# Performance work log

Hardware: AMD Instinct MI355X
Metric: run time of the kernel (lower is better)

Reference implementation:

```python
import jax, jax.numpy as jnp
import numpy as np

EPS = 1e-06
H = 25  # num heads


def _rmsnorm(x, w, eps=EPS):
    # normalize over last dim in float32, as in the torch module
    xf = x.astype(jnp.float32)
    var = jnp.mean(xf * xf, axis=-1, keepdims=True)
    return (w * (xf * jax.lax.rsqrt(var + eps))).astype(x.dtype)


def setup_inputs() -> dict:
    key = jax.random.key(0)
    ks = jax.random.split(key, 4)
    B, N, C = 8, 1025, 3200
    x = jax.random.normal(ks[0], (B, N, C), dtype=jnp.float32)
    qkv_w = jax.random.normal(ks[1], (C, 3 * C), dtype=jnp.float32) * (C ** -0.5)
    qkv_b = jnp.zeros((3 * C,), dtype=jnp.float32)
    q_norm_w = jnp.ones((C,), dtype=jnp.float32)
    k_norm_w = jnp.ones((C,), dtype=jnp.float32)
    proj_w = jax.random.normal(ks[2], (C, C), dtype=jnp.float32) * (C ** -0.5)
    proj_b = jnp.zeros((C,), dtype=jnp.float32)
    return {"x": x, "qkv_w": qkv_w, "qkv_b": qkv_b, "q_norm_w": q_norm_w,
            "k_norm_w": k_norm_w, "proj_w": proj_w, "proj_b": proj_b}


def reference(x, qkv_w, qkv_b, q_norm_w, k_norm_w, proj_w, proj_b):
    B, N, C = x.shape
    D = C // H
    scale = D ** -0.5
    qkv = x @ qkv_w + qkv_b                      # [B, N, 3C]
    q, k, v = jnp.split(qkv, 3, axis=-1)         # each [B, N, C]
    # QK RMSNorm is over the FULL embed_dim (heads flattened), per source.
    q = _rmsnorm(q, q_norm_w)
    k = _rmsnorm(k, k_norm_w)
    q = q.reshape(B, N, H, D)
    k = k.reshape(B, N, H, D)
    v = v.reshape(B, N, H, D)
    attn = jnp.einsum('bqhd,bkhd->bhqk', q * scale, k)   # [B, H, N, N]
    attn = jax.nn.softmax(attn, axis=-1)
    out = jnp.einsum('bhqk,bkhd->bqhd', attn, v).reshape(B, N, C)
    return out @ proj_w + proj_b
```

## Files before the change

kernel.cpp:

```cpp
#include <hip/hip_runtime.h>
#include <hip/hip_bf16.h>
#include <math.h>

#define B_ 8
#define N_ 1025
#define C_ 3200
#define H_ 25
#define D_ 128
#define M_ (B_ * N_)
#define C3_ (3 * C_)

typedef unsigned short u16;
typedef unsigned int u32;
typedef short bf16x8 __attribute__((ext_vector_type(8)));
typedef float f32x4 __attribute__((ext_vector_type(4)));

__device__ inline void load_lds16(const void* g, void* s) {
    __builtin_amdgcn_global_load_lds(
        (const __attribute__((address_space(1))) void*)g,
        (__attribute__((address_space(3))) void*)s, 16, 0, 0);
}

__device__ inline void split_pair(float x0, float x1, u32& hpk, u32& lpk) {
    __hip_bfloat162 h2 = __float22bfloat162_rn(float2{x0, x1});
    union { __hip_bfloat162 b; u32 u; } cv; cv.b = h2;
    u32 h = cv.u;
    float hf0 = __uint_as_float(h << 16);
    float hf1 = __uint_as_float(h & 0xFFFF0000u);
    __hip_bfloat162 l2 = __float22bfloat162_rn(float2{x0 - hf0, x1 - hf1});
    union { __hip_bfloat162 b; u32 u; } cl; cl.b = l2;
    hpk = h; lpk = cl.u;
}

__device__ inline void split1(float x, u16& h, u16& l) {
    union { __hip_bfloat16 b; u16 u; } ch, cl;
    ch.b = __float2bfloat16(x);
    float hf = __uint_as_float(((u32)ch.u) << 16);
    cl.b = __float2bfloat16(x - hf);
    h = ch.u; l = cl.u;
}

__global__ __launch_bounds__(256) void convert_split(
    const float4* __restrict__ in, uint2* __restrict__ hi,
    uint2* __restrict__ lo, int n4)
{
    int i = blockIdx.x * 256 + threadIdx.x;
    if (i < n4) {
        float4 v = in[i];
        u32 h0, l0, h1, l1;
        split_pair(v.x, v.y, h0, l0);
        split_pair(v.z, v.w, h1, l1);
        hi[i] = make_uint2(h0, h1);
        lo[i] = make_uint2(l0, l1);
    }
}

__global__ __launch_bounds__(256) void convert_tsplit(
    const float* __restrict__ in, u16* __restrict__ hi, u16* __restrict__ lo,
    int K, int Nn)
{
    __shared__ float T[32][33];
    const int tid = threadIdx.x;
    const int nb = blockIdx.x * 32, kb = blockIdx.y * 32;
    #pragma unroll
    for (int p = 0; p < 4; ++p) {
        int k = p * 8 + (tid >> 5), n = tid & 31;
        T[k][n] = in[(size_t)(kb + k) * Nn + nb + n];
    }
    __syncthreads();
    const int nn = tid >> 3, k0 = (tid & 7) * 4;
    u32 h0, l0, h1, l1;
    split_pair(T[k0][nn], T[k0 + 1][nn], h0, l0);
    split_pair(T[k0 + 2][nn], T[k0 + 3][nn], h1, l1);
    size_t o = (size_t)(nb + nn) * K + kb + k0;
    *(uint2*)&hi[o] = make_uint2(h0, h1);
    *(uint2*)&lo[o] = make_uint2(l0, l1);
}

__global__ __launch_bounds__(256) void gemm_bf16split(
    const u16* __restrict__ Ah, const u16* __restrict__ Al,
    const u16* __restrict__ Bh, const u16* __restrict__ Bl,
    const float* __restrict__ bias, float* __restrict__ Cc,
    int M, int N)
{
    __shared__ u16 As_h[4][128][8];
    __shared__ u16 As_l[4][128][8];
    __shared__ u16 Bs_h[4][128][8];
    __shared__ u16 Bs_l[4][128][8];

    const int tid  = threadIdx.x;
    const int lane = tid & 63;
    const int w    = tid >> 6;
    const int wm   = w & 1, wn = w >> 1;
    const int lr = lane & 15, lg = lane >> 4;

    const int gX   = gridDim.x;
    const int nwg  = gX * gridDim.y;
    const int orig = blockIdx.y * gX + blockIdx.x;
    const int q8 = nwg >> 3, r8 = nwg & 7;
    const int xcd = orig & 7, oi = orig >> 3;
    const int wg = (xcd < r8 ? xcd * (q8 + 1)
                             : r8 * (q8 + 1) + (xcd - r8) * q8) + oi;
    const int rowBase = (wg / gX) * 128;
    const int colBase = (wg % gX) * 128;

    f32x4 acc[4][4] = {};

    for (int k0 = 0; k0 < C_; k0 += 32) {
        #pragma unroll
        for (int p = 0; p < 2; ++p) {
            int c   = p * 256 + tid;
            int row = c & 127, kc = c >> 7;
            int ldsOff = (p * 256 + w * 64) * 8;
            int ar = rowBase + row; if (ar >= M) ar = M - 1;
            size_t aoff = (size_t)ar * C_ + k0 + kc * 8;
            size_t boff = (size_t)(colBase + row) * C_ + k0 + kc * 8;
            load_lds16(Ah + aoff, (u16*)As_h + ldsOff);
            load_lds16(Al + aoff, (u16*)As_l + ldsOff);
            load_lds16(Bh + boff, (u16*)Bs_h + ldsOff);
            load_lds16(Bl + boff, (u16*)Bs_l + ldsOff);
        }
        __syncthreads();

        bf16x8 ah[4], al[4], bh[4], bl[4];
        #pragma unroll
        for (int i = 0; i < 4; ++i) {
            ah[i] = *(const bf16x8*)&As_h[lg][wm * 64 + i * 16 + lr][0];
            al[i] = *(const bf16x8*)&As_l[lg][wm * 64 + i * 16 + lr][0];
            bh[i] = *(const bf16x8*)&Bs_h[lg][wn * 64 + i * 16 + lr][0];
            bl[i] = *(const bf16x8*)&Bs_l[lg][wn * 64 + i * 16 + lr][0];
        }

        #pragma unroll
        for (int j = 0; j < 4; ++j)
            #pragma unroll
            for (int i = 0; i < 4; ++i)
                acc[i][j] = __builtin_amdgcn_mfma_f32_16x16x32_bf16(
                    ah[i], bh[j], acc[i][j], 0, 0, 0);
        #pragma unroll
        for (int j = 0; j < 4; ++j)
            #pragma unroll
            for (int i = 0; i < 4; ++i)
                acc[i][j] = __builtin_amdgcn_mfma_f32_16x16x32_bf16(
                    al[i], bh[j], acc[i][j], 0, 0, 0);
        #pragma unroll
        for (int j = 0; j < 4; ++j)
            #pragma unroll
            for (int i = 0; i < 4; ++i)
                acc[i][j] = __builtin_amdgcn_mfma_f32_16x16x32_bf16(
                    ah[i], bl[j], acc[i][j], 0, 0, 0);
        __syncthreads();
    }

    #pragma unroll
    for (int i = 0; i < 4; ++i) {
        #pragma unroll
        for (int j = 0; j < 4; ++j) {
            int gc = colBase + wn * 64 + j * 16 + lr;
            float bv = bias[gc];
            #pragma unroll
            for (int r = 0; r < 4; ++r) {
                int gr = rowBase + wm * 64 + i * 16 + lg * 4 + r;
                if (gr < M) Cc[(size_t)gr * N + gc] = acc[i][j][r] + bv;
            }
        }
    }
}

__global__ __launch_bounds__(256) void gemm_split(
    const float* __restrict__ A, const float* __restrict__ Bm,
    const float* __restrict__ bias, float* __restrict__ Cc,
    int M, int N)
{
    __shared__ u16  As_hi[128 * 32];
    __shared__ u16  As_lo[128 * 32];
    __shared__ float Bf[32 * 128];

    const int tid  = threadIdx.x;
    const int lane = tid & 63;
    const int w    = tid >> 6;
    const int wm   = w & 1, wn = w >> 1;
    const int rowBase = blockIdx.y * 128;
    const int colBase = blockIdx.x * 128;
    const int lr = lane & 15, lg = lane >> 4;

    const int ar = tid >> 3;
    const int ak = (tid & 7) * 4;

    f32x4 acc[4][4] = {};

    for (int k0 = 0; k0 < C_; k0 += 32) {
        #pragma unroll
        for (int p = 0; p < 4; ++p) {
            int c = p * 256 + tid;
            const float* g = Bm + (size_t)(k0 + (c >> 5)) * N
                                + colBase + (c & 31) * 4;
            load_lds16(g, &Bf[(p * 256 + w * 64) * 4]);
        }
        #pragma unroll
        for (int p = 0; p < 4; ++p) {
            int r  = p * 32 + ar;
            int gr = rowBase + r; if (gr >= M) gr = M - 1;
            float4 a4 = *(const float4*)(A + (size_t)gr * C_ + k0 + ak);
            u32 h0, h1, l0, l1;
            split_pair(a4.x, a4.y, h0, l0);
            split_pair(a4.z, a4.w, h1, l1);
            *(uint2*)&As_hi[r * 32 + ak] = make_uint2(h0, h1);
            *(uint2*)&As_lo[r * 32 + ak] = make_uint2(l0, l1);
        }
        __syncthreads();

        bf16x8 ah[4], al[4];
        #pragma unroll
        for (int i = 0; i < 4; ++i) {
            ah[i] = *(const bf16x8*)&As_hi[(wm * 64 + i * 16 + lr) * 32 + lg * 8];
            al[i] = *(const bf16x8*)&As_lo[(wm * 64 + i * 16 + lr) * 32 + lg * 8];
        }
        #pragma unroll
        for (int j = 0; j < 4; ++j) {
            const float* bp = &Bf[(lg * 8) * 128 + wn * 64 + j * 16 + lr];
            union { u32 u[4]; bf16x8 v; } BH, BL;
            split_pair(bp[0 * 128], bp[1 * 128], BH.u[0], BL.u[0]);
            split_pair(bp[2 * 128], bp[3 * 128], BH.u[1], BL.u[1]);
            split_pair(bp[4 * 128], bp[5 * 128], BH.u[2], BL.u[2]);
            split_pair(bp[6 * 128], bp[7 * 128], BH.u[3], BL.u[3]);
            #pragma unroll
            for (int i = 0; i < 4; ++i)
                acc[i][j] = __builtin_amdgcn_mfma_f32_16x16x32_bf16(
                    ah[i], BH.v, acc[i][j], 0, 0, 0);
            #pragma unroll
            for (int i = 0; i < 4; ++i)
                acc[i][j] = __builtin_amdgcn_mfma_f32_16x16x32_bf16(
                    al[i], BH.v, acc[i][j], 0, 0, 0);
            #pragma unroll
            for (int i = 0; i < 4; ++i)
                acc[i][j] = __builtin_amdgcn_mfma_f32_16x16x32_bf16(
                    ah[i], BL.v, acc[i][j], 0, 0, 0);
        }
        __syncthreads();
    }

    #pragma unroll
    for (int i = 0; i < 4; ++i) {
        #pragma unroll
        for (int j = 0; j < 4; ++j) {
            int gc = colBase + wn * 64 + j * 16 + lr;
            float bv = bias[gc];
            #pragma unroll
            for (int r = 0; r < 4; ++r) {
                int gr = rowBase + wm * 64 + i * 16 + lg * 4 + r;
                if (gr < M) Cc[(size_t)gr * N + gc] = acc[i][j][r] + bv;
            }
        }
    }
}

__global__ __launch_bounds__(256) void rmsnorm_kernel(
    float* __restrict__ qkv, const float* __restrict__ qw,
    const float* __restrict__ kw)
{
    const int row   = blockIdx.x >> 1;
    const int which = blockIdx.x & 1;
    float* p = qkv + (size_t)row * C3_ + which * C_;
    const float* w = which ? kw : qw;
    const int tid = threadIdx.x;

    float ss = 0.f;
    for (int i = tid; i < C_ / 4; i += 256) {
        float4 v = ((const float4*)p)[i];
        ss += v.x * v.x + v.y * v.y + v.z * v.z + v.w * v.w;
    }
    #pragma unroll
    for (int off = 32; off; off >>= 1) ss += __shfl_down(ss, off);

    __shared__ float wsum[4];
    __shared__ float stot;
    if ((tid & 63) == 0) wsum[tid >> 6] = ss;
    __syncthreads();
    if (tid == 0) stot = wsum[0] + wsum[1] + wsum[2] + wsum[3];
    __syncthreads();

    const float scale = rsqrtf(stot / (float)C_ + 1e-6f);
    for (int i = tid; i < C_ / 4; i += 256) {
        float4 v  = ((const float4*)p)[i];
        float4 wv = ((const float4*)w)[i];
        v.x *= scale * wv.x; v.y *= scale * wv.y;
        v.z *= scale * wv.z; v.w *= scale * wv.w;
        ((float4*)p)[i] = v;
    }
}

__global__ __launch_bounds__(256, 2) void flash_mfma(
    const float* __restrict__ qkv, float* __restrict__ attn_out)
{
    __shared__ u16 Kh[4][32][32];
    __shared__ u16 Kl[4][32][32];
    __shared__ u16 Vth[128][40];
    __shared__ u16 Vtl[128][40];
    __shared__ u16 Ph[4][16][40];
    __shared__ u16 Pl[4][16][40];

    const int b   = blockIdx.z;
    const int h   = blockIdx.y;
    const int q0  = blockIdx.x * 64;
    const int tid = threadIdx.x;
    const int lane = tid & 63;
    const int w    = tid >> 6;
    const int lr = lane & 15, lg = lane >> 4;
    const float scale = 0.088388347648318447f;

    bf16x8 qh[4], ql[4];
    {
        int qr = q0 + w * 16 + lr;
        if (qr >= N_) qr = N_ - 1;
        const float* qp = qkv + (size_t)(b * N_ + qr) * C3_ + h * D_;
        #pragma unroll
        for (int c = 0; c < 4; ++c) {
            float4 x0 = *(const float4*)(qp + c * 32 + lg * 8);
            float4 x1 = *(const float4*)(qp + c * 32 + lg * 8 + 4);
            union { u32 u[4]; bf16x8 v; } Hq, Lq;
            split_pair(x0.x * scale, x0.y * scale, Hq.u[0], Lq.u[0]);
            split_pair(x0.z * scale, x0.w * scale, Hq.u[1], Lq.u[1]);
            split_pair(x1.x * scale, x1.y * scale, Hq.u[2], Lq.u[2]);
            split_pair(x1.z * scale, x1.w * scale, Hq.u[3], Lq.u[3]);
            qh[c] = Hq.v; ql[c] = Lq.v;
        }
    }

    const float* Kbase = qkv + (size_t)b * N_ * C3_ + C_ + h * D_;
    const float* Vbase = qkv + (size_t)b * N_ * C3_ + 2 * C_ + h * D_;

    const int skr = tid >> 3;
    const int skd = (tid & 7) * 16;
    const int svk = (tid & 15) * 2;
    const int svd = (tid >> 4) * 4;

    float4 kg[4], vg[2][2];

    auto stage_load = [&](int kt) {
        int kk = kt * 32 + skr;
        if (kk < N_) {
            const float* p = Kbase + (size_t)kk * C3_ + skd;
            kg[0] = *(const float4*)(p + 0);
            kg[1] = *(const float4*)(p + 4);
            kg[2] = *(const float4*)(p + 8);
            kg[3] = *(const float4*)(p + 12);
        } else {
            kg[0] = kg[1] = kg[2] = kg[3] = make_float4(0.f, 0.f, 0.f, 0.f);
        }
        #pragma unroll
        for (int r = 0; r < 2; ++r) {
            int vk = kt * 32 + svk + r;
            if (vk < N_) {
                const float* p = Vbase + (size_t)vk * C3_ + svd;
                vg[0][r] = *(const float4*)(p);
                vg[1][r] = *(const float4*)(p + 64);
            } else {
                vg[0][r] = make_float4(0.f, 0.f, 0.f, 0.f);
                vg[1][r] = make_float4(0.f, 0.f, 0.f, 0.f);
            }
        }
    };

    auto stage_store = [&]() {
        #pragma unroll
        for (int i = 0; i < 4; ++i) {
            int d = skd + i * 4;
            int c = d >> 5, dd = d & 31;
            u32 h0, l0, h1, l1;
            split_pair(kg[i].x, kg[i].y, h0, l0);
            split_pair(kg[i].z, kg[i].w, h1, l1);
            *(uint2*)&Kh[c][skr][dd] = make_uint2(h0, h1);
            *(uint2*)&Kl[c][skr][dd] = make_uint2(l0, l1);
        }
        #pragma unroll
        for (int half = 0; half < 2; ++half) {
            float a0[4] = { vg[half][0].x, vg[half][0].y, vg[half][0].z, vg[half][0].w };
            float a1[4] = { vg[half][1].x, vg[half][1].y, vg[half][1].z, vg[half][1].w };
            #pragma unroll
            for (int i = 0; i < 4; ++i) {
                int d = svd + half * 64 + i;
                u32 hp, lp;
                split_pair(a0[i], a1[i], hp, lp);
                *(u32*)&Vth[d][svk] = hp;
                *(u32*)&Vtl[d][svk] = lp;
            }
        }
    };

    f32x4 oacc[8] = {};
    float m[4]    = { -INFINITY, -INFINITY, -INFINITY, -INFINITY };
    float lsum[4] = { 0.f, 0.f, 0.f, 0.f };

    const int nkt = (N_ + 31) / 32;
    stage_load(0);
    for (int kt = 0; kt < nkt; ++kt) {
        __syncthreads();
        stage_store();
        __syncthreads();
        if (kt + 1 < nkt) stage_load(kt + 1);

        f32x4 s0 = {}, s1 = {};
        #pragma unroll
        for (int c = 0; c < 4; ++c) {
            bf16x8 kh0 = *(const bf16x8*)&Kh[c][lr][lg * 8];
            bf16x8 kl0 = *(const bf16x8*)&Kl[c][lr][lg * 8];
            bf16x8 kh1 = *(const bf16x8*)&Kh[c][16 + lr][lg * 8];
            bf16x8 kl1 = *(const bf16x8*)&Kl[c][16 + lr][lg * 8];
            s0 = __builtin_amdgcn_mfma_f32_16x16x32_bf16(qh[c], kh0, s0, 0, 0, 0);
            s0 = __builtin_amdgcn_mfma_f32_16x16x32_bf16(ql[c], kh0, s0, 0, 0, 0);
            s0 = __builtin_amdgcn_mfma_f32_16x16x32_bf16(qh[c], kl0, s0, 0, 0, 0);
            s1 = __builtin_amdgcn_mfma_f32_16x16x32_bf16(qh[c], kh1, s1, 0, 0, 0);
            s1 = __builtin_amdgcn_mfma_f32_16x16x32_bf16(ql[c], kh1, s1, 0, 0, 0);
            s1 = __builtin_amdgcn_mfma_f32_16x16x32_bf16(qh[c], kl1, s1, 0, 0, 0);
        }

        const int kb = kt * 32;
        const bool v0 = (kb + lr) < N_;
        const bool v1 = (kb + 16 + lr) < N_;
        #pragma unroll
        for (int r = 0; r < 4; ++r) {
            if (!v0) s0[r] = -INFINITY;
            if (!v1) s1[r] = -INFINITY;
        }

        #pragma unroll
        for (int r = 0; r < 4; ++r) {
            float mt = fmaxf(s0[r], s1[r]);
            mt = fmaxf(mt, __shfl_xor(mt, 1));
            mt = fmaxf(mt, __shfl_xor(mt, 2));
            mt = fmaxf(mt, __shfl_xor(mt, 4));
            mt = fmaxf(mt, __shfl_xor(mt, 8));
            float mn = fmaxf(m[r], mt);
            float al = __expf(m[r] - mn);
            m[r] = mn;
            float p0 = __expf(s0[r] - mn);
            float p1 = __expf(s1[r] - mn);
            float ls = p0 + p1;
            ls += __shfl_xor(ls, 1);
            ls += __shfl_xor(ls, 2);
            ls += __shfl_xor(ls, 4);
            ls += __shfl_xor(ls, 8);
            lsum[r] = lsum[r] * al + ls;
            #pragma unroll
            for (int dt = 0; dt < 8; ++dt) oacc[dt][r] *= al;

            u16 hh, ll;
            split1(p0, hh, ll);
            Ph[w][lg * 4 + r][lr] = hh;
            Pl[w][lg * 4 + r][lr] = ll;
            split1(p1, hh, ll);
            Ph[w][lg * 4 + r][16 + lr] = hh;
            Pl[w][lg * 4 + r][16 + lr] = ll;
        }

        bf16x8 pah = *(const bf16x8*)&Ph[w][lr][lg * 8];
        bf16x8 pal = *(const bf16x8*)&Pl[w][lr][lg * 8];
        #pragma unroll
        for (int dt = 0; dt < 8; ++dt) {
            bf16x8 vh = *(const bf16x8*)&Vth[dt * 16 + lr][lg * 8];
            bf16x8 vl = *(const bf16x8*)&Vtl[dt * 16 + lr][lg * 8];
            oacc[dt] = __builtin_amdgcn_mfma_f32_16x16x32_bf16(pah, vh, oacc[dt], 0, 0, 0);
            oacc[dt] = __builtin_amdgcn_mfma_f32_16x16x32_bf16(pal, vh, oacc[dt], 0, 0, 0);
            oacc[dt] = __builtin_amdgcn_mfma_f32_16x16x32_bf16(pah, vl, oacc[dt], 0, 0, 0);
        }
    }

    #pragma unroll
    for (int r = 0; r < 4; ++r) {
        int q = q0 + w * 16 + lg * 4 + r;
        if (q < N_) {
            float inv = 1.f / lsum[r];
            float* op = attn_out + (size_t)(b * N_ + q) * C_ + h * D_ + lr;
            #pragma unroll
            for (int dt = 0; dt < 8; ++dt) op[dt * 16] = oacc[dt][r] * inv;
        }
    }
}

extern "C" void kernel_launch(void* const* d_in, const int* in_sizes, int n_in,
                              void* d_out, int out_size, void* d_ws, size_t ws_size,
                              hipStream_t stream)
{
    const float* x        = (const float*)d_in[0];
    const float* qkv_w    = (const float*)d_in[1];
    const float* qkv_b    = (const float*)d_in[2];
    const float* q_norm_w = (const float*)d_in[3];
    const float* k_norm_w = (const float*)d_in[4];
    const float* proj_w   = (const float*)d_in[5];
    const float* proj_b   = (const float*)d_in[6];
    float* out = (float*)d_out;

    const size_t fQ = (size_t)M_ * C3_;
    const size_t fA = (size_t)M_ * C_;
    const size_t uW = (size_t)C3_ * C_;

    float* qkv      = (float*)d_ws;
    float* attn_out = qkv + fQ;

    const size_t need = (fQ + fA) * 4 + fA * 2 * 2 + uW * 2 * 2;

    dim3 blk(256);

    if (ws_size >= need) {
        u16* xh = (u16*)(attn_out + fA);
        u16* xl = xh + fA;
        u16* wh = xl + fA;
        u16* wl = wh + uW;

        const int n4 = (int)(fA / 4);

        convert_split<<<dim3((n4 + 255) / 256), blk, 0, stream>>>(
            (const float4*)x, (uint2*)xh, (uint2*)xl, n4);
        convert_tsplit<<<dim3(C3_ / 32, C_ / 32), blk, 0, stream>>>(
            qkv_w, wh, wl, C_, C3_);

        gemm_bf16split<<<dim3(C3_ / 128, (M_ + 127) / 128), blk, 0, stream>>>(
            xh, xl, wh, wl, qkv_b, qkv, M_, C3_);

        rmsnorm_kernel<<<dim3(M_ * 2), blk, 0, stream>>>(qkv, q_norm_w, k_norm_w);

        flash_mfma<<<dim3((N_ + 63) / 64, H_, B_), blk, 0, stream>>>(qkv, attn_out);

        convert_split<<<dim3((n4 + 255) / 256), blk, 0, stream>>>(
            (const float4*)attn_out, (uint2*)xh, (uint2*)xl, n4);
        convert_tsplit<<<dim3(C_ / 32, C_ / 32), blk, 0, stream>>>(
            proj_w, wh, wl, C_, C_);

        gemm_bf16split<<<dim3(C_ / 128, (M_ + 127) / 128), blk, 0, stream>>>(
            xh, xl, wh, wl, proj_b, out, M_, C_);
    } else {
        gemm_split<<<dim3(C3_ / 128, (M_ + 127) / 128), blk, 0, stream>>>(
            x, qkv_w, qkv_b, qkv, M_, C3_);
        rmsnorm_kernel<<<dim3(M_ * 2), blk, 0, stream>>>(qkv, q_norm_w, k_norm_w);
        flash_mfma<<<dim3((N_ + 63) / 64, H_, B_), blk, 0, stream>>>(qkv, attn_out);
        gemm_split<<<dim3(C_ / 128, (M_ + 127) / 128), blk, 0, stream>>>(
            attn_out, proj_w, proj_b, out, M_, C_);
    }
}
```

Measured before the change: 3.999 ms.

## Fuse input bf16 split into QKV GEMM and emit split attention output directly

The QKV GEMM now reads fp32 x and splits it into hi/lo bf16 in registers while loading it into LDS, prefetching the next k-slice, which removes the separate convert pass over x. The QKV weight is converted and multiplied in three C-wide chunks so the workspace only needs one CxC split buffer. The flash kernel writes the hi/lo bf16 split of its output directly, dropping the fp32 attention buffer and its convert kernel. The proj weight split reuses the start of the qkv workspace, which is dead after attention, and the small-workspace fallback path is removed. The cost is more launches, x being re-read and re-split three times, and a hard dependence on a minimum workspace size.

```diff
diff --git a/kernel.cpp b/kernel.cpp
--- a/kernel.cpp
+++ b/kernel.cpp
@@ -40,24 +40,9 @@
     h = ch.u; l = cl.u;
 }
 
-__global__ __launch_bounds__(256) void convert_split(
-    const float4* __restrict__ in, uint2* __restrict__ hi,
-    uint2* __restrict__ lo, int n4)
-{
-    int i = blockIdx.x * 256 + threadIdx.x;
-    if (i < n4) {
-        float4 v = in[i];
-        u32 h0, l0, h1, l1;
-        split_pair(v.x, v.y, h0, l0);
-        split_pair(v.z, v.w, h1, l1);
-        hi[i] = make_uint2(h0, h1);
-        lo[i] = make_uint2(l0, l1);
-    }
-}
-
 __global__ __launch_bounds__(256) void convert_tsplit(
     const float* __restrict__ in, u16* __restrict__ hi, u16* __restrict__ lo,
-    int K, int Nn)
+    int K, int Nn, int strideN)
 {
     __shared__ float T[32][33];
     const int tid = threadIdx.x;
@@ -65,7 +50,7 @@
     #pragma unroll
     for (int p = 0; p < 4; ++p) {
         int k = p * 8 + (tid >> 5), n = tid & 31;
-        T[k][n] = in[(size_t)(kb + k) * Nn + nb + n];
+        T[k][n] = in[(size_t)(kb + k) * strideN + nb + n];
     }
     __syncthreads();
     const int nn = tid >> 3, k0 = (tid & 7) * 4;
@@ -77,11 +62,11 @@
     *(uint2*)&lo[o] = make_uint2(l0, l1);
 }
 
-__global__ __launch_bounds__(256) void gemm_bf16split(
-    const u16* __restrict__ Ah, const u16* __restrict__ Al,
+__global__ __launch_bounds__(256) void gemm_asplit(
+    const float* __restrict__ A,
     const u16* __restrict__ Bh, const u16* __restrict__ Bl,
     const float* __restrict__ bias, float* __restrict__ Cc,
-    int M, int N)
+    int M, int N, int ldc)
 {
     __shared__ u16 As_h[4][128][8];
     __shared__ u16 As_l[4][128][8];
@@ -104,12 +89,124 @@
     const int rowBase = (wg / gX) * 128;
     const int colBase = (wg % gX) * 128;
 
+    const int arow = tid >> 1;
+    const int akh  = (tid & 1) * 16;
+    const int kc0  = akh >> 3;
+    int gr0 = rowBase + arow; if (gr0 >= M) gr0 = M - 1;
+    const float* aptr = A + (size_t)gr0 * C_ + akh;
+
     f32x4 acc[4][4] = {};
 
+    float4 a0 = *(const float4*)(aptr + 0);
+    float4 a1 = *(const float4*)(aptr + 4);
+    float4 a2 = *(const float4*)(aptr + 8);
+    float4 a3 = *(const float4*)(aptr + 12);
+
     for (int k0 = 0; k0 < C_; k0 += 32) {
         #pragma unroll
         for (int p = 0; p < 2; ++p) {
-            int c   = p * 256 + tid;
+            int c = p * 256 + tid;
+            int row = c & 127, kc = c >> 7;
+            int ldsOff = (p * 256 + w * 64) * 8;
+            size_t boff = (size_t)(colBase + row) * C_ + k0 + kc * 8;
+            load_lds16(Bh + boff, (u16*)Bs_h + ldsOff);
+            load_lds16(Bl + boff, (u16*)Bs_l + ldsOff);
+        }
+        u32 h0,h1,h2,h3,h4,h5,h6,h7, l0,l1,l2,l3,l4,l5,l6,l7;
+        split_pair(a0.x, a0.y, h0, l0); split_pair(a0.z, a0.w, h1, l1);
+        split_pair(a1.x, a1.y, h2, l2); split_pair(a1.z, a1.w, h3, l3);
+        split_pair(a2.x, a2.y, h4, l4); split_pair(a2.z, a2.w, h5, l5);
+        split_pair(a3.x, a3.y, h6, l6); split_pair(a3.z, a3.w, h7, l7);
+        *(uint4*)&As_h[kc0][arow][0]     = make_uint4(h0, h1, h2, h3);
+        *(uint4*)&As_h[kc0 + 1][arow][0] = make_uint4(h4, h5, h6, h7);
+        *(uint4*)&As_l[kc0][arow][0]     = make_uint4(l0, l1, l2, l3);
+        *(uint4*)&As_l[kc0 + 1][arow][0] = make_uint4(l4, l5, l6, l7);
+        if (k0 + 32 < C_) {
+            const float* ap = aptr + k0 + 32;
+            a0 = *(const float4*)(ap + 0);
+            a1 = *(const float4*)(ap + 4);
+            a2 = *(const float4*)(ap + 8);
+            a3 = *(const float4*)(ap + 12);
+        }
+        __syncthreads();
+
+        bf16x8 ah[4], al[4], bh[4], bl[4];
+        #pragma unroll
+        for (int i = 0; i < 4; ++i) {
+            ah[i] = *(const bf16x8*)&As_h[lg][wm * 64 + i * 16 + lr][0];
+            al[i] = *(const bf16x8*)&As_l[lg][wm * 64 + i * 16 + lr][0];
+            bh[i] = *(const bf16x8*)&Bs_h[lg][wn * 64 + i * 16 + lr][0];
+            bl[i] = *(const bf16x8*)&Bs_l[lg][wn * 64 + i * 16 + lr][0];
+        }
+        #pragma unroll
+        for (int j = 0; j < 4; ++j)
+            #pragma unroll
+            for (int i = 0; i < 4; ++i)
+                acc[i][j] = __builtin_amdgcn_mfma_f32_16x16x32_bf16(
+                    ah[i], bh[j], acc[i][j], 0, 0, 0);
+        #pragma unroll
+        for (int j = 0; j < 4; ++j)
+            #pragma unroll
+            for (int i = 0; i < 4; ++i)
+                acc[i][j] = __builtin_amdgcn_mfma_f32_16x16x32_bf16(
+                    al[i], bh[j], acc[i][j], 0, 0, 0);
+        #pragma unroll
+        for (int j = 0; j < 4; ++j)
+            #pragma unroll
+            for (int i = 0; i < 4; ++i)
+                acc[i][j] = __builtin_amdgcn_mfma_f32_16x16x32_bf16(
+                    ah[i], bl[j], acc[i][j], 0, 0, 0);
+        __syncthreads();
+    }
+
+    #pragma unroll
+    for (int i = 0; i < 4; ++i) {
+        #pragma unroll
+        for (int j = 0; j < 4; ++j) {
+            int gc = colBase + wn * 64 + j * 16 + lr;
+            float bv = bias[gc];
+            #pragma unroll
+            for (int r = 0; r < 4; ++r) {
+                int gr = rowBase + wm * 64 + i * 16 + lg * 4 + r;
+                if (gr < M) Cc[(size_t)gr * ldc + gc] = acc[i][j][r] + bv;
+            }
+        }
+    }
+}
+
+__global__ __launch_bounds__(256) void gemm_bf16split(
+    const u16* __restrict__ Ah, const u16* __restrict__ Al,
+    const u16* __restrict__ Bh, const u16* __restrict__ Bl,
+    const float* __restrict__ bias, float* __restrict__ Cc,
+    int M, int N, int ldc)
+{
+    __shared__ u16 As_h[4][128][8];
+    __shared__ u16 As_l[4][128][8];
+    __shared__ u16 Bs_h[4][128][8];
+    __shared__ u16 Bs_l[4][128][8];
+
+    const int tid  = threadIdx.x;
+    const int lane = tid & 63;
+    const int w    = tid >> 6;
+    const int wm   = w & 1, wn = w >> 1;
+    const int lr = lane & 15, lg = lane >> 4;
+
+    const int gX   = gridDim.x;
+    const int nwg  = gX * gridDim.y;
+    const int orig = blockIdx.y * gX + blockIdx.x;
+    const int q8 = nwg >> 3, r8 = nwg & 7;
+    const int xcd = orig & 7, oi = orig >> 3;
+    const int wg = (xcd < r8 ? xcd * (q8 + 1)
+                             : r8 * (q8 + 1) + (xcd - r8) * q8) + oi;
+    const int rowBase = (wg / gX) * 128;
+    const int colBase = (wg % gX) * 128;
+
+    f32x4 acc[4][4] = {};
+
+    for (int k0 = 0; k0 < C_; k0 += 32) {
+        #pragma unroll
+        for (int p = 0; p < 2; ++p) {
+            int c = p * 256 + tid;
             int row = c & 127, kc = c >> 7;
             int ldsOff = (p * 256 + w * 64) * 8;
             int ar = rowBase + row; if (ar >= M) ar = M - 1;
@@ -130,7 +227,6 @@
             bh[i] = *(const bf16x8*)&Bs_h[lg][wn * 64 + i * 16 + lr][0];
             bl[i] = *(const bf16x8*)&Bs_l[lg][wn * 64 + i * 16 + lr][0];
         }
-
         #pragma unroll
         for (int j = 0; j < 4; ++j)
             #pragma unroll
@@ -161,95 +257,7 @@
             #pragma unroll
             for (int r = 0; r < 4; ++r) {
                 int gr = rowBase + wm * 64 + i * 16 + lg * 4 + r;
-                if (gr < M) Cc[(size_t)gr * N + gc] = acc[i][j][r] + bv;
-            }
-        }
-    }
-}
-
-__global__ __launch_bounds__(256) void gemm_split(
-    const float* __restrict__ A, const float* __restrict__ Bm,
-    const float* __restrict__ bias, float* __restrict__ Cc,
-    int M, int N)
-{
-    __shared__ u16  As_hi[128 * 32];
-    __shared__ u16  As_lo[128 * 32];
-    __shared__ float Bf[32 * 128];
-
-    const int tid  = threadIdx.x;
-    const int lane = tid & 63;
-    const int w    = tid >> 6;
-    const int wm   = w & 1, wn = w >> 1;
-    const int rowBase = blockIdx.y * 128;
-    const int colBase = blockIdx.x * 128;
-    const int lr = lane & 15, lg = lane >> 4;
-
-    const int ar = tid >> 3;
-    const int ak = (tid & 7) * 4;
-
-    f32x4 acc[4][4] = {};
-
-    for (int k0 = 0; k0 < C_; k0 += 32) {
-        #pragma unroll
-        for (int p = 0; p < 4; ++p) {
-            int c = p * 256 + tid;
-            const float* g = Bm + (size_t)(k0 + (c >> 5)) * N
-                                + colBase + (c & 31) * 4;
-            load_lds16(g, &Bf[(p * 256 + w * 64) * 4]);
-        }
-        #pragma unroll
-        for (int p = 0; p < 4; ++p) {
-            int r  = p * 32 + ar;
-            int gr = rowBase + r; if (gr >= M) gr = M - 1;
-            float4 a4 = *(const float4*)(A + (size_t)gr * C_ + k0 + ak);
-            u32 h0, h1, l0, l1;
-            split_pair(a4.x, a4.y, h0, l0);
-            split_pair(a4.z, a4.w, h1, l1);
-            *(uint2*)&As_hi[r * 32 + ak] = make_uint2(h0, h1);
-            *(uint2*)&As_lo[r * 32 + ak] = make_uint2(l0, l1);
-        }
-        __syncthreads();
-
-        bf16x8 ah[4], al[4];
-        #pragma unroll
-        for (int i = 0; i < 4; ++i) {
-            ah[i] = *(const bf16x8*)&As_hi[(wm * 64 + i * 16 + lr) * 32 + lg * 8];
-            al[i] = *(const bf16x8*)&As_lo[(wm * 64 + i * 16 + lr) * 32 + lg * 8];
-        }
-        #pragma unroll
-        for (int j = 0; j < 4; ++j) {
-            const float* bp = &Bf[(lg * 8) * 128 + wn * 64 + j * 16 + lr];
-            union { u32 u[4]; bf16x8 v; } BH, BL;
-            split_pair(bp[0 * 128], bp[1 * 128], BH.u[0], BL.u[0]);
-            split_pair(bp[2 * 128], bp[3 * 128], BH.u[1], BL.u[1]);
-            split_pair(bp[4 * 128], bp[5 * 128], BH.u[2], BL.u[2]);
-            split_pair(bp[6 * 128], bp[7 * 128], BH.u[3], BL.u[3]);
-            #pragma unroll
-            for (int i = 0; i < 4; ++i)
-                acc[i][j] = __builtin_amdgcn_mfma_f32_16x16x32_bf16(
-                    ah[i], BH.v, acc[i][j], 0, 0, 0);
-            #pragma unroll
-            for (int i = 0; i < 4; ++i)
-                acc[i][j] = __builtin_amdgcn_mfma_f32_16x16x32_bf16(
-                    al[i], BH.v, acc[i][j], 0, 0, 0);
-            #pragma unroll
-            for (int i = 0; i < 4; ++i)
-                acc[i][j] = __builtin_amdgcn_mfma_f32_16x16x32_bf16(
-                    ah[i], BL.v, acc[i][j], 0, 0, 0);
-        }
-        __syncthreads();
-    }
-
-    #pragma unroll
-    for (int i = 0; i < 4; ++i) {
-        #pragma unroll
-        for (int j = 0; j < 4; ++j) {
-            int gc = colBase + wn * 64 + j * 16 + lr;
-            float bv = bias[gc];
-            #pragma unroll
-            for (int r = 0; r < 4; ++r) {
-                int gr = rowBase + wm * 64 + i * 16 + lg * 4 + r;
-                if (gr < M) Cc[(size_t)gr * N + gc] = acc[i][j][r] + bv;
+                if (gr < M) Cc[(size_t)gr * ldc + gc] = acc[i][j][r] + bv;
             }
         }
     }
@@ -291,7 +299,7 @@
 }
 
 __global__ __launch_bounds__(256, 2) void flash_mfma(
-    const float* __restrict__ qkv, float* __restrict__ attn_out)
+    const float* __restrict__ qkv, u16* __restrict__ aoh, u16* __restrict__ aol)
 {
     __shared__ u16 Kh[4][32][32];
     __shared__ u16 Kl[4][32][32];
@@ -471,9 +479,14 @@
         int q = q0 + w * 16 + lg * 4 + r;
         if (q < N_) {
             float inv = 1.f / lsum[r];
-            float* op = attn_out + (size_t)(b * N_ + q) * C_ + h * D_ + lr;
-            #pragma unroll
-            for (int dt = 0; dt < 8; ++dt) op[dt * 16] = oacc[dt][r] * inv;
+            size_t base = (size_t)(b * N_ + q) * C_ + h * D_ + lr;
+            #pragma unroll
+            for (int dt = 0; dt < 8; ++dt) {
+                u16 hh, ll;
+                split1(oacc[dt][r] * inv, hh, ll);
+                aoh[base + dt * 16] = hh;
+                aol[base + dt * 16] = ll;
+            }
         }
     }
 }
@@ -493,48 +506,31 @@
 
     const size_t fQ = (size_t)M_ * C3_;
     const size_t fA = (size_t)M_ * C_;
-    const size_t uW = (size_t)C3_ * C_;
-
-    float* qkv      = (float*)d_ws;
-    float* attn_out = qkv + fQ;
-
-    const size_t need = (fQ + fA) * 4 + fA * 2 * 2 + uW * 2 * 2;
+    const size_t wC = (size_t)C_ * C_;
+
+    float* qkv = (float*)d_ws;
+    u16*   R   = (u16*)(qkv + fQ);
 
     dim3 blk(256);
 
-    if (ws_size >= need) {
-        u16* xh = (u16*)(attn_out + fA);
-        u16* xl = xh + fA;
-        u16* wh = xl + fA;
-        u16* wl = wh + uW;
-
-        const int n4 = (int)(fA / 4);
-
-        convert_split<<<dim3((n4 + 255) / 256), blk, 0, stream>>>(
-            (const float4*)x, (uint2*)xh, (uint2*)xl, n4);
-        convert_tsplit<<<dim3(C3_ / 32, C_ / 32), blk, 0, stream>>>(
-            qkv_w, wh, wl, C_, C3_);
-
-        gemm_bf16split<<<dim3(C3_ / 128, (M_ + 127) / 128), blk, 0, stream>>>(
-            xh, xl, wh, wl, qkv_b, qkv, M_, C3_);
-
-        rmsnorm_kernel<<<dim3(M_ * 2), blk, 0, stream>>>(qkv, q_norm_w, k_norm_w);
-
-        flash_mfma<<<dim3((N_ + 63) / 64, H_, B_), blk, 0, stream>>>(qkv, attn_out);
-
-        convert_split<<<dim3((n4 + 255) / 256), blk, 0, stream>>>(
-            (const float4*)attn_out, (uint2*)xh, (uint2*)xl, n4);
+    u16* wh = R;
+    u16* wl = wh + wC;
+    for (int j = 0; j < 3; ++j) {
         convert_tsplit<<<dim3(C_ / 32, C_ / 32), blk, 0, stream>>>(
-            proj_w, wh, wl, C_, C_);
-
-        gemm_bf16split<<<dim3(C_ / 128, (M_ + 127) / 128), blk, 0, stream>>>(
-            xh, xl, wh, wl, proj_b, out, M_, C_);
-    } else {
-        gemm_split<<<dim3(C3_ / 128, (M_ + 127) / 128), blk, 0, stream>>>(
-            x, qkv_w, qkv_b, qkv, M_, C3_);
-        rmsnorm_kernel<<<dim3(M_ * 2), blk, 0, stream>>>(qkv, q_norm_w, k_norm_w);
-        flash_mfma<<<dim3((N_ + 63) / 64, H_, B_), blk, 0, stream>>>(qkv, attn_out);
-        gemm_split<<<dim3(C_ / 128, (M_ + 127) / 128), blk, 0, stream>>>(
-            attn_out, proj_w, proj_b, out, M_, C_);
-    }
-}
+            qkv_w + (size_t)j * C_, wh, wl, C_, C_, C3_);
+        gemm_asplit<<<dim3(C_ / 128, (M_ + 127) / 128), blk, 0, stream>>>(
+            x, wh, wl, qkv_b + j * C_, qkv + (size_t)j * C_, M_, C_, C3_);
+    }
+
+    rmsnorm_kernel<<<dim3(M_ * 2), blk, 0, stream>>>(qkv, q_norm_w, k_norm_w);
+    u16* aoh = R;
+    u16* aol = R + fA;
+    flash_mfma<<<dim3((N_ + 63) / 64, H_, B_), blk, 0, stream>>>(qkv, aoh, aol);
+
+    u16* ph = (u16*)d_ws;
+    u16* pl = ph + wC;
+    convert_tsplit<<<dim3(C_ / 32, C_ / 32), blk, 0, stream>>>(
+        proj_w, ph, pl, C_, C_, C_);
+    gemm_bf16split<<<dim3(C_ / 128, (M_ + 127) / 128), blk, 0, stream>>>(
+        aoh, aol, ph, pl, proj_b, out, M_, C_, C_);
+}
```

Result: slower. 4.305 ms (+7.7%).
